# Kernel tuning notes

Hardware: AMD Instinct MI355X
Metric: run time of the kernel (lower is better)

Reference implementation:

```python
import jax, jax.numpy as jnp
import numpy as np

LOSS_WEIGHT = 1.0


def setup_inputs() -> dict:
    key = jax.random.key(0)
    k1, k2 = jax.random.split(key)
    source = jax.random.normal(k1, (8, 4096, 3), dtype=jnp.float32)
    target = jax.random.normal(k2, (8, 4096, 3), dtype=jnp.float32)
    return {"source": source, "target": target}


def reference(source, target):
    # Pairwise Euclidean distances via the Gram-matrix identity (same math as torch.cdist):
    # d(i,j)^2 = ||s_i||^2 + ||t_j||^2 - 2 <s_i, t_j>
    s2 = jnp.sum(source * source, axis=-1)  # [B, N]
    t2 = jnp.sum(target * target, axis=-1)  # [B, M]
    cross = jnp.einsum("bnd,bmd->bnm", source, target)  # [B, N, M]
    d2 = s2[:, :, None] + t2[:, None, :] - 2.0 * cross
    dists = jnp.sqrt(jnp.maximum(d2, 0.0))  # [B, N, M]
    term1 = jnp.mean(jnp.min(dists, axis=2), axis=1)  # source -> nearest target
    term2 = jnp.mean(jnp.min(dists, axis=1), axis=1)  # target -> nearest source
    return LOSS_WEIGHT * (jnp.mean(term1) + jnp.mean(term2))
```

## Files before the change

### kernel.cpp

```cpp
#include <hip/hip_runtime.h>

#define BB 8
#define NN 4096
#define BLK 256
#define RPT 4
#define ROWS 128
#define SLICES 8
#define JSL (NN/SLICES)
#define NBLK (2*BB*(NN/ROWS))

__global__ __launch_bounds__(BLK) void cd_main(const float* __restrict__ src,
                                               const float* __restrict__ tgt,
                                               float* __restrict__ partial) {
    __shared__ float4 tl[NN];
    __shared__ float pmin[SLICES * ROWS];
    __shared__ float bsum[4];
    const int dir = blockIdx.z;
    const float* Sp = dir ? tgt : src;
    const float* Tp = dir ? src : tgt;
    const int b   = blockIdx.y;
    const int rt  = blockIdx.x;
    const int tid = threadIdx.x;

    const float* tb = Tp + (size_t)b * NN * 3;
    for (int k = tid; k < NN; k += BLK) {
        float x = tb[3*k], y = tb[3*k+1], z = tb[3*k+2];
        tl[k] = make_float4(x, y, z, 0.5f*(x*x + y*y + z*z));
    }

    const float* sb = Sp + (size_t)b * NN * 3;
    const int sub   = tid & 31;
    const int slice = tid >> 5;
    const int rowBase = rt * ROWS;
    float nx[RPT], ny[RPT], nz[RPT], q[RPT];
#pragma unroll
    for (int r = 0; r < RPT; ++r) {
        int row = rowBase + sub + 32*r;
        float x = sb[3*row], y = sb[3*row+1], z = sb[3*row+2];
        nx[r] = -x; ny[r] = -y; nz[r] = -z;
        q[r] = 0.5f*(x*x + y*y + z*z);
    }
    __syncthreads();

    float m0[RPT], m1[RPT];
#pragma unroll
    for (int r = 0; r < RPT; ++r) { m0[r] = 1.0e30f; m1[r] = 1.0e30f; }

    const float4* tp = tl + slice * JSL;
#pragma unroll 2
    for (int j = 0; j < JSL; j += 2) {
        float4 t0 = tp[j];
        float4 t1 = tp[j+1];
#pragma unroll
        for (int r = 0; r < RPT; ++r) {
            float a0 = fmaf(nx[r], t0.x, fmaf(ny[r], t0.y, fmaf(nz[r], t0.z, t0.w)));
            float a1 = fmaf(nx[r], t1.x, fmaf(ny[r], t1.y, fmaf(nz[r], t1.z, t1.w)));
            m0[r] = fminf(m0[r], a0);
            m1[r] = fminf(m1[r], a1);
        }
    }

#pragma unroll
    for (int r = 0; r < RPT; ++r)
        pmin[slice*ROWS + sub + 32*r] = fminf(m0[r], m1[r]) + q[r];
    __syncthreads();

    float dsum = 0.0f;
    if (tid < ROWS) {
        float v = pmin[tid];
#pragma unroll
        for (int s = 1; s < SLICES; ++s) v = fminf(v, pmin[s*ROWS + tid]);
        v = fmaxf(v, 0.0f);
        dsum = sqrtf(2.0f * v);
    }
#pragma unroll
    for (int o = 32; o > 0; o >>= 1) dsum += __shfl_down(dsum, o, 64);
    if ((tid & 63) == 0) bsum[tid >> 6] = dsum;
    __syncthreads();
    if (tid == 0)
        partial[((size_t)dir*BB + b)*32 + rt] = bsum[0] + bsum[1] + bsum[2] + bsum[3];
}

__global__ __launch_bounds__(512) void cd_final(const float* __restrict__ partial,
                                                float* __restrict__ out) {
    __shared__ float ps[8];
    float v = partial[threadIdx.x];
#pragma unroll
    for (int o = 32; o > 0; o >>= 1) v += __shfl_down(v, o, 64);
    if ((threadIdx.x & 63) == 0) ps[threadIdx.x >> 6] = v;
    __syncthreads();
    if (threadIdx.x == 0) {
        float t = 0.0f;
#pragma unroll
        for (int w = 0; w < 8; ++w) t += ps[w];
        out[0] = t * (1.0f / (float)(BB * NN));
    }
}

extern "C" void kernel_launch(void* const* d_in, const int* in_sizes, int n_in,
                              void* d_out, int out_size, void* d_ws, size_t ws_size,
                              hipStream_t stream) {
    const float* src = (const float*)d_in[0];
    const float* tgt = (const float*)d_in[1];
    float* partial = (float*)d_ws;
    float* out = (float*)d_out;

    dim3 grid(NN/ROWS, BB, 2);
    cd_main<<<grid, BLK, 0, stream>>>(src, tgt, partial);
    cd_final<<<1, 512, 0, stream>>>(partial, out);
}
```

Baseline: 80.65 us.

## Widen blocks to 512 threads with 8 rows per thread and padded LDS slices

Doubles the block size and the rows held per thread, and splits the target set into 32 slices of 128 points. Each slice is stored in LDS with one float4 of padding per slice to spread bank accesses. Per-slice minima are combined with cross-lane shuffles inside each wave before a smaller shared-memory reduction, and the two min accumulators are merged into one. The aim is more register reuse of each LDS target load and less LDS traffic, at the cost of higher register pressure and a longer dependent fminf chain.

```diff
diff --git a/kernel.cpp b/kernel.cpp
--- a/kernel.cpp
+++ b/kernel.cpp
@@ -2,19 +2,21 @@
 
 #define BB 8
 #define NN 4096
-#define BLK 256
-#define RPT 4
+#define BLK 512
+#define RPT 8
 #define ROWS 128
-#define SLICES 8
+#define SLICES 32
 #define JSL (NN/SLICES)
+#define PADJ (JSL + 1)
+#define NWAVE (BLK/64)
 #define NBLK (2*BB*(NN/ROWS))
 
-__global__ __launch_bounds__(BLK) void cd_main(const float* __restrict__ src,
-                                               const float* __restrict__ tgt,
-                                               float* __restrict__ partial) {
-    __shared__ float4 tl[NN];
-    __shared__ float pmin[SLICES * ROWS];
-    __shared__ float bsum[4];
+__global__ __launch_bounds__(BLK, 4) void cd_main(const float* __restrict__ src,
+                                                  const float* __restrict__ tgt,
+                                                  float* __restrict__ partial) {
+    __shared__ float4 tl[SLICES * PADJ];
+    __shared__ float pmin[NWAVE * ROWS];
+    __shared__ float bsum[NWAVE];
     const int dir = blockIdx.z;
     const float* Sp = dir ? tgt : src;
     const float* Tp = dir ? src : tgt;
@@ -25,28 +27,28 @@
     const float* tb = Tp + (size_t)b * NN * 3;
     for (int k = tid; k < NN; k += BLK) {
         float x = tb[3*k], y = tb[3*k+1], z = tb[3*k+2];
-        tl[k] = make_float4(x, y, z, 0.5f*(x*x + y*y + z*z));
+        tl[(k >> 7) * PADJ + (k & (JSL - 1))] = make_float4(x, y, z, 0.5f*(x*x + y*y + z*z));
     }
 
     const float* sb = Sp + (size_t)b * NN * 3;
-    const int sub   = tid & 31;
-    const int slice = tid >> 5;
+    const int sub   = tid & 15;
+    const int slice = tid >> 4;
     const int rowBase = rt * ROWS;
     float nx[RPT], ny[RPT], nz[RPT], q[RPT];
 #pragma unroll
     for (int r = 0; r < RPT; ++r) {
-        int row = rowBase + sub + 32*r;
+        int row = rowBase + sub + 16*r;
         float x = sb[3*row], y = sb[3*row+1], z = sb[3*row+2];
         nx[r] = -x; ny[r] = -y; nz[r] = -z;
         q[r] = 0.5f*(x*x + y*y + z*z);
     }
     __syncthreads();
 
-    float m0[RPT], m1[RPT];
+    float m[RPT];
 #pragma unroll
-    for (int r = 0; r < RPT; ++r) { m0[r] = 1.0e30f; m1[r] = 1.0e30f; }
+    for (int r = 0; r < RPT; ++r) m[r] = 1.0e30f;
 
-    const float4* tp = tl + slice * JSL;
+    const float4* tp = tl + slice * PADJ;
 #pragma unroll 2
     for (int j = 0; j < JSL; j += 2) {
         float4 t0 = tp[j];
@@ -55,21 +57,30 @@
         for (int r = 0; r < RPT; ++r) {
             float a0 = fmaf(nx[r], t0.x, fmaf(ny[r], t0.y, fmaf(nz[r], t0.z, t0.w)));
             float a1 = fmaf(nx[r], t1.x, fmaf(ny[r], t1.y, fmaf(nz[r], t1.z, t1.w)));
-            m0[r] = fminf(m0[r], a0);
-            m1[r] = fminf(m1[r], a1);
+            m[r] = fminf(m[r], fminf(a0, a1));
         }
     }
 
 #pragma unroll
-    for (int r = 0; r < RPT; ++r)
-        pmin[slice*ROWS + sub + 32*r] = fminf(m0[r], m1[r]) + q[r];
+    for (int r = 0; r < RPT; ++r) {
+        float v = m[r];
+        v = fminf(v, __shfl_xor(v, 16, 64));
+        v = fminf(v, __shfl_xor(v, 32, 64));
+        m[r] = v + q[r];
+    }
+    const int wid = tid >> 6;
+    if ((tid & 63) < 16) {
+#pragma unroll
+        for (int r = 0; r < RPT; ++r)
+            pmin[wid*ROWS + sub + 16*r] = m[r];
+    }
     __syncthreads();
 
     float dsum = 0.0f;
     if (tid < ROWS) {
         float v = pmin[tid];
 #pragma unroll
-        for (int s = 1; s < SLICES; ++s) v = fminf(v, pmin[s*ROWS + tid]);
+        for (int s = 1; s < NWAVE; ++s) v = fminf(v, pmin[s*ROWS + tid]);
         v = fmaxf(v, 0.0f);
         dsum = sqrtf(2.0f * v);
     }
@@ -77,8 +88,12 @@
     for (int o = 32; o > 0; o >>= 1) dsum += __shfl_down(dsum, o, 64);
     if ((tid & 63) == 0) bsum[tid >> 6] = dsum;
     __syncthreads();
-    if (tid == 0)
-        partial[((size_t)dir*BB + b)*32 + rt] = bsum[0] + bsum[1] + bsum[2] + bsum[3];
+    if (tid == 0) {
+        float t = 0.0f;
+#pragma unroll
+        for (int w = 0; w < NWAVE; ++w) t += bsum[w];
+        partial[((size_t)dir*BB + b)*32 + rt] = t;
+    }
 }
 
 __global__ __launch_bounds__(512) void cd_final(const float* __restrict__ partial,
```

Result: faster. 78.29 us (-2.9%).
